# Kernel optimization log

Measured on AMD Instinct MI355X. Metric: run time of the kernel, lower is better.

The kernel has to match this reference:

```python
import jax, jax.numpy as jnp
import numpy as np

N_SP, N_SPAT = 20000, 10000
E_SS, E_BIP, E_SP = 160000, 320000, 320000
H, C = 4, 64  # GAT heads / per-head channels (hidden_channels=64, concat=False)
EPS = 1e-6


def _gat(xs, xd, row, col, ea, Ws, Wd, a_s, a_d, a_e, We, b, num_dst, heads, ch, self_loops, concat):
    # PyG GATConv with edge_dim: linear -> per-head additive attention -> softmax over incoming edges -> scatter-add
    hs = (xs @ Ws).reshape(-1, heads, ch)          # [Ns,H,C]
    hd = (xd @ Wd).reshape(-1, heads, ch)          # [Nd,H,C]
    al_s = jnp.sum(hs * a_s, -1)                   # [Ns,H]
    al_d = jnp.sum(hd * a_d, -1)                   # [Nd,H]
    if self_loops:
        # add_self_loops with fill_value='mean': loop edge_attr = mean of incoming edge_attr per node
        cnt = jax.ops.segment_sum(jnp.ones((row.shape[0],), ea.dtype), col, num_dst)
        loop_ea = jax.ops.segment_sum(ea, col, num_dst) / jnp.maximum(cnt, 1.0)[:, None]
        loops = jnp.arange(num_dst, dtype=row.dtype)
        row = jnp.concatenate([row, loops])
        col = jnp.concatenate([col, loops])
        ea = jnp.concatenate([ea, loop_ea], 0)
    he = (ea @ We).reshape(-1, heads, ch)          # [E,H,C]
    al = jax.nn.leaky_relu(al_s[row] + al_d[col] + jnp.sum(he * a_e, -1), 0.2)  # [E,H]
    m = jax.ops.segment_max(al, col, num_segments=num_dst)
    ex = jnp.exp(al - m[col])
    den = jax.ops.segment_sum(ex, col, num_segments=num_dst)
    alpha = ex / (den[col] + 1e-16)
    out = jax.ops.segment_sum(hs[row] * alpha[..., None], col, num_segments=num_dst)  # [Nd,H,C]
    out = out.reshape(num_dst, heads * ch) if concat else out.mean(1)
    return out + b


def setup_inputs() -> dict:
    key = jax.random.key(0)
    ks = iter(jax.random.split(key, 64))
    f = lambda shape: jax.random.normal(next(ks), shape, jnp.float32)
    w = lambda shape: f(shape) / np.sqrt(shape[0])
    inp = {}
    inp['species_x_mean'] = f((N_SP, 32))
    inp['species_x_std'] = jax.random.uniform(next(ks), (N_SP, 32), jnp.float32)
    inp['traits_nanmask'] = jax.random.bernoulli(next(ks), 0.4, (N_SP, 32))
    inp['species_x_gen'] = f((N_SP, 64))
    inp['species_x_phylo'] = f((N_SP, 128))
    inp['spatial_x'] = f((N_SPAT, 12))
    inp['spatial_global_data'] = f((N_SPAT, 4))
    ei = lambda e, ns, nd: jnp.stack([jax.random.randint(next(ks), (e,), 0, ns, jnp.int32),
                                      jax.random.randint(next(ks), (e,), 0, nd, jnp.int32)])
    inp['ss_edge_index'] = ei(E_SS, N_SPAT, N_SPAT)
    inp['ss_edge_attr'] = jax.random.uniform(next(ks), (E_SS, 1), jnp.float32)
    inp['bip_edge_index'] = ei(E_BIP, N_SPAT, N_SP)
    inp['bip_edge_attr'] = jax.random.uniform(next(ks), (E_BIP, 1), jnp.float32)
    inp['sp_edge_index'] = ei(E_SP, N_SP, N_SP)
    inp['sp_edge_attr'] = jax.random.uniform(next(ks), (E_SP, 1), jnp.float32)
    # GAT conv params: space_gnn (sg0, sg1), species_gnn (pg0, pg1)
    for nm, din in [('sg0', 16), ('sg1', 64), ('pg0', 128), ('pg1', 64)]:
        inp[nm + '_W'] = w((din, H * C))
        inp[nm + '_as'] = f((H, C)) * 0.1
        inp[nm + '_ad'] = f((H, C)) * 0.1
        inp[nm + '_ae'] = f((H, C)) * 0.1
        inp[nm + '_We'] = w((1, H * C))
        inp[nm + '_b'] = jnp.zeros((C,), jnp.float32)
    # bipartite GATConv: heads=1, concat=True, src dim=hidden=64, dst dim=in_gen+in_phylo=192
    inp['bp_Ws'] = w((64, 64))
    inp['bp_Wd'] = w((192, 64))
    inp['bp_as'] = f((1, 64)) * 0.1
    inp['bp_ad'] = f((1, 64)) * 0.1
    inp['bp_ae'] = f((1, 64)) * 0.1
    inp['bp_We'] = w((1, 64))
    inp['bp_b'] = jnp.zeros((64,), jnp.float32)
    inp['sl_W'] = w((288, 64))
    inp['sl_b'] = jnp.zeros((64,), jnp.float32)
    inp['fc_W'] = w((64, 64))
    inp['fc_b'] = jnp.zeros((64,), jnp.float32)
    return inp


def reference(species_x_mean, species_x_std, traits_nanmask, species_x_gen, species_x_phylo,
              spatial_x, spatial_global_data, ss_edge_index, ss_edge_attr, bip_edge_index,
              bip_edge_attr, sp_edge_index, sp_edge_attr,
              sg0_W, sg0_as, sg0_ad, sg0_ae, sg0_We, sg0_b,
              sg1_W, sg1_as, sg1_ad, sg1_ae, sg1_We, sg1_b,
              pg0_W, pg0_as, pg0_ad, pg0_ae, pg0_We, pg0_b,
              pg1_W, pg1_as, pg1_ad, pg1_ae, pg1_We, pg1_b,
              bp_Ws, bp_Wd, bp_as, bp_ad, bp_ae, bp_We, bp_b,
              sl_W, sl_b, fc_W, fc_b):
    # inference path: no trait masking -> visibility = observed mask
    vis = (~traits_nanmask).astype(jnp.float32)
    sp_in = jnp.concatenate([species_x_mean, species_x_std, vis, species_x_gen, species_x_phylo], 1)
    sp_in = jax.nn.relu(sp_in @ sl_W + sl_b)                      # [N_SP,64]
    # spatial GNN (2 GATConv layers, heads=4, concat=False, self loops)
    h = jnp.concatenate([spatial_x, spatial_global_data], 1)      # [N_SPAT,16]
    r, c = ss_edge_index[0], ss_edge_index[1]
    h = jax.nn.relu(_gat(h, h, r, c, ss_edge_attr, sg0_W, sg0_W, sg0_as, sg0_ad, sg0_ae, sg0_We, sg0_b, N_SPAT, H, C, True, False))
    h = jax.nn.relu(_gat(h, h, r, c, ss_edge_attr, sg1_W, sg1_W, sg1_as, sg1_ad, sg1_ae, sg1_We, sg1_b, N_SPAT, H, C, True, False))
    # bipartite spatial->species GATConv (heads=1, concat=True, no self loops)
    part = jnp.concatenate([species_x_gen, species_x_phylo], 1)   # [N_SP,192]
    br, bc = bip_edge_index[0], bip_edge_index[1]
    sts = jax.nn.relu(_gat(h, part, br, bc, bip_edge_attr, bp_Ws, bp_Wd, bp_as, bp_ad, bp_ae, bp_We, bp_b, N_SP, 1, 64, False, True))
    # species GNN (2 GATConv layers)
    x = jnp.concatenate([sts, sp_in], 1)                          # [N_SP,128]
    pr, pc = sp_edge_index[0], sp_edge_index[1]
    x = jax.nn.relu(_gat(x, x, pr, pc, sp_edge_attr, pg0_W, pg0_W, pg0_as, pg0_ad, pg0_ae, pg0_We, pg0_b, N_SP, H, C, True, False))
    x = jax.nn.relu(_gat(x, x, pr, pc, sp_edge_attr, pg1_W, pg1_W, pg1_as, pg1_ad, pg1_ae, pg1_We, pg1_b, N_SP, H, C, True, False))
    ms = x @ fc_W + fc_b                                          # [N_SP, 2*out]
    mean, log_std = jnp.split(ms, 2, axis=-1)
    std = jax.nn.softplus(log_std) + EPS
    return mean, std
```

## Files before the change

### kernel.cpp

```cpp
#include <hip/hip_runtime.h>
#include <hip/hip_bf16.h>

#define NSP   20000
#define NSPAT 10000
#define ESS   160000
#define EBIP  320000
#define ESP   320000

static inline int cdiv_host(long a, long b) { return (int)((a + b - 1) / b); }

__device__ __forceinline__ float wave_red_sum(float p) {
#pragma unroll
  for (int m = 32; m >= 1; m >>= 1) p += __shfl_xor(p, m, 64);
  return p;
}
__device__ __forceinline__ float bf2f(unsigned short u) {
  return __uint_as_float(((unsigned int)u) << 16);
}
__device__ __forceinline__ unsigned short f2bf(float f) {
  unsigned int u = __float_as_uint(f);
  unsigned int r = (u + 0x7FFF + ((u >> 16) & 1)) >> 16;
  return (unsigned short)r;
}

__global__ void count3_kernel(
    const int* c1, int E1, int* cp1, int* rnk1, int n1,
    const int* c2, int E2, int* cp2, int* rnk2, int n2,
    const int* c3, int E3, int* cp3, int* rnk3, int n3,
    const unsigned int* __restrict__ mask, int* __restrict__ flag) {
  int b = blockIdx.x, t = threadIdx.x;
  if (b == gridDim.x - 1) {
    if (t < 64) {
      unsigned int w0 = mask[t], w1 = mask[t + 64], w2 = mask[t + 128], w3 = mask[t + 192];
      bool ai = (w0 <= 1u) && (w1 <= 1u) && (w2 <= 1u) && (w3 <= 1u);
      auto okf = [](unsigned int w) { return w == 0u || w == 0x3f800000u; };
      bool af = okf(w0) && okf(w1) && okf(w2) && okf(w3);
      unsigned long long bi = __ballot(ai), bf = __ballot(af);
      if (t == 0) *flag = (bi == ~0ull) ? 0 : ((bf == ~0ull) ? 2 : 1);
    }
    return;
  }
  int i = b * 256 + t;
  int total = E1 + E2 + E3;
  if (i >= total) return;
  int p = (i >> 8) & 7;
  if (i < E1) {
    int d = c1[i]; rnk1[i] = atomicAdd(&cp1[p * n1 + d], 1);
  } else if (i < E1 + E2) {
    int j = i - E1;
    int d = c2[j]; rnk2[j] = atomicAdd(&cp2[p * n2 + d], 1);
  } else {
    int j = i - E1 - E2;
    int d = c3[j]; rnk3[j] = atomicAdd(&cp3[p * n3 + d], 1);
  }
}

__global__ void merge3_kernel(int* cp1, int* c1, int n1,
                              int* cp2, int* c2, int n2,
                              int* cp3, int* c3, int n3) {
  int i = blockIdx.x * blockDim.x + threadIdx.x;
  int total = n1 + n2 + n3;
  if (i >= total) return;
  int *cp, *c; int n, d;
  if (i < n1) { cp = cp1; c = c1; n = n1; d = i; }
  else if (i < n1 + n2) { cp = cp2; c = c2; n = n2; d = i - n1; }
  else { cp = cp3; c = c3; n = n3; d = i - n1 - n2; }
  int s = 0;
#pragma unroll
  for (int p = 0; p < 8; ++p) { int t = cp[p * n + d]; cp[p * n + d] = s; s += t; }
  c[d] = s;
}

__global__ __launch_bounds__(1024) void scan3_kernel(
    const int* cntA, int nA, int* ptrA,
    const int* cntB, int nB, int* ptrB,
    const int* cntC, int nC, int* ptrC) {
  const int* cnt; int n; int* ptr;
  if (blockIdx.x == 0) { cnt = cntA; n = nA; ptr = ptrA; }
  else if (blockIdx.x == 1) { cnt = cntB; n = nB; ptr = ptrB; }
  else { cnt = cntC; n = nC; ptr = ptrC; }
  __shared__ int part[1024];
  int t = threadIdx.x;
  int ch = (n + 1023) / 1024;
  int beg = t * ch, end = min(beg + ch, n);
  int s = 0;
  for (int i = beg; i < end; ++i) s += cnt[i];
  part[t] = s;
  __syncthreads();
  for (int off = 1; off < 1024; off <<= 1) {
    int v = (t >= off) ? part[t - off] : 0;
    __syncthreads();
    part[t] += v;
    __syncthreads();
  }
  int run = (t == 0) ? 0 : part[t - 1];
  for (int i = beg; i < end; ++i) { ptr[i] = run; run += cnt[i]; }
  if (t == 1023) ptr[n] = part[1023];
}

struct DoteArgs { const float* We[5]; const float* ae[5]; float* dotes; };
struct PrepArgs {
  const float* mean; const float* stdv; const void* mask; const int* flag;
  const float* sx; const float* sg; float* spc96; float* h0;
};

__global__ void scatter3x_kernel(
    const int* r1, const int* c1, const float* e1, int E1, const int* p1, const int* cp1, const int* k1, int n1, int* s1, float* a1,
    const int* r2, const int* c2, const float* e2, int E2, const int* p2, const int* cp2, const int* k2, int n2, int* s2, float* a2,
    const int* r3, const int* c3, const float* e3, int E3, const int* p3, const int* cp3, const int* k3, int n3, int* s3, float* a3,
    DoteArgs da, PrepArgs pa) {
  const int NB_SC = (ESS + EBIP + ESP + 255) / 256;
  int b = blockIdx.x, t = threadIdx.x;
  if (b < NB_SC) {
    int i = b * 256 + t;
    if (i >= E1 + E2 + E3) return;
    int p = (i >> 8) & 7;
    if (i < E1) {
      int d = c1[i];
      int pos = p1[d] + cp1[p * n1 + d] + k1[i];
      s1[pos] = r1[i]; a1[pos] = e1[i];
    } else if (i < E1 + E2) {
      int j = i - E1;
      int d = c2[j];
      int pos = p2[d] + cp2[p * n2 + d] + k2[j];
      s2[pos] = r2[j]; a2[pos] = e2[j];
    } else {
      int j = i - E1 - E2;
      int d = c3[j];
      int pos = p3[d] + cp3[p * n3 + d] + k3[j];
      s3[pos] = r3[j]; a3[pos] = e3[j];
    }
  } else if (b < NB_SC + 5) {
    int lb = b - NB_SC;
    int n = (lb == 2) ? 64 : 256;
    if (t < n) {
      float p = wave_red_sum(da.We[lb][t] * da.ae[lb][t]);
      if ((t & 63) == 0) da.dotes[lb * 4 + (t >> 6)] = p;
    }
  } else {
    const long totA = (long)NSP * 96;
    const long totB = (long)NSPAT * 16;
    long i = (long)(b - NB_SC - 5) * 256 + t;
    if (i >= totA + totB) return;
    int mode = *pa.flag;
    if (i < totA) {
      int n = (int)(i / 96), c = (int)(i % 96);
      float v;
      if (c < 32) v = pa.mean[(long)n * 32 + c];
      else if (c < 64) v = pa.stdv[(long)n * 32 + (c - 32)];
      else {
        long j = (long)n * 32 + (c - 64);
        int mv;
        if (mode == 0) mv = ((const int*)pa.mask)[j];
        else if (mode == 2) mv = (((const float*)pa.mask)[j] != 0.0f);
        else mv = (int)((const unsigned char*)pa.mask)[j];
        v = mv ? 0.f : 1.f;
      }
      pa.spc96[i] = v;
    } else {
      long k = i - totA;
      int n = (int)(k / 16), c = (int)(k % 16);
      pa.h0[k] = (c < 12) ? pa.sx[(long)n * 12 + c] : pa.sg[(long)n * 4 + (c - 12)];
    }
  }
}

struct XSrc { const float* p[5]; int w[5]; int n; };
struct PJob {
  XSrc xs; int M, K;
  const float* W; const float* bias; int mode;
  const float* a_s; const float* a_d;
  float* al_s; float* al_d;
  float* Y; float* Y2;
};
struct LeafArgs {
  const int* ss_ptr; const float* ss_cea; float* ss_lea;
  const int* pp_ptr; const float* pp_cea; float* pp_lea;
};

__device__ __forceinline__ void proj64_body(const PJob& J, int bid,
                                            float* wl, float* xl) {
  constexpr int KC = 32;
  constexpr int BR = 32;
  constexpr int KCP = 36;
  int t = threadIdx.x;
  long row0 = (long)bid * BR;
  if (row0 >= J.M) return;
  int cg = t & 15, rg = t >> 4;
  int c0 = cg * 4;

  float acc[2][4];
#pragma unroll
  for (int r = 0; r < 2; ++r)
#pragma unroll
    for (int j = 0; j < 4; ++j) acc[r][j] = 0.f;

  for (int k0 = 0; k0 < J.K; k0 += KC) {
    int seg = 0; int base = 0;
    while (k0 >= base + J.xs.w[seg]) { base += J.xs.w[seg]; ++seg; }
    const float* Xp = J.xs.p[seg];
    int stride = J.xs.w[seg];
    int kloc = k0 - base;

    __syncthreads();
    {
      const float4* ws = (const float4*)(J.W + (long)k0 * 64);
      float4* wd = (float4*)wl;
      wd[t] = ws[t];
      wd[t + 256] = ws[t + 256];
    }
    {
      int r = t >> 3, kq = (t & 7) * 4;
      long rr = row0 + r; if (rr >= J.M) rr = J.M - 1;
      float4 v = *(const float4*)(Xp + rr * stride + kloc + kq);
      *(float4*)(xl + r * KCP + kq) = v;
    }
    __syncthreads();

    for (int kg = 0; kg < KC; kg += 4) {
      float4 w0 = *(const float4*)(wl + (kg + 0) * 64 + c0);
      float4 w1 = *(const float4*)(wl + (kg + 1) * 64 + c0);
      float4 w2 = *(const float4*)(wl + (kg + 2) * 64 + c0);
      float4 w3 = *(const float4*)(wl + (kg + 3) * 64 + c0);
#pragma unroll
      for (int r = 0; r < 2; ++r) {
        float4 xv = *(const float4*)(xl + (rg * 2 + r) * KCP + kg);
        acc[r][0] = fmaf(xv.x, w0.x, acc[r][0]);
        acc[r][1] = fmaf(xv.x, w0.y, acc[r][1]);
        acc[r][2] = fmaf(xv.x, w0.z, acc[r][2]);
        acc[r][3] = fmaf(xv.x, w0.w, acc[r][3]);
        acc[r][0] = fmaf(xv.y, w1.x, acc[r][0]);
        acc[r][1] = fmaf(xv.y, w1.y, acc[r][1]);
        acc[r][2] = fmaf(xv.y, w1.z, acc[r][2]);
        acc[r][3] = fmaf(xv.y, w1.w, acc[r][3]);
        acc[r][0] = fmaf(xv.z, w2.x, acc[r][0]);
        acc[r][1] = fmaf(xv.z, w2.y, acc[r][1]);
        acc[r][2] = fmaf(xv.z, w2.z, acc[r][2]);
        acc[r][3] = fmaf(xv.z, w2.w, acc[r][3]);
        acc[r][0] = fmaf(xv.w, w3.x, acc[r][0]);
        acc[r][1] = fmaf(xv.w, w3.y, acc[r][1]);
        acc[r][2] = fmaf(xv.w, w3.z, acc[r][2]);
        acc[r][3] = fmaf(xv.w, w3.w, acc[r][3]);
      }
    }
  }

  float4 bv = make_float4(0.f, 0.f, 0.f, 0.f);
  float4 asv = make_float4(0.f, 0.f, 0.f, 0.f);
  float4 adv = make_float4(0.f, 0.f, 0.f, 0.f);
  if (J.bias) bv = *(const float4*)(J.bias + c0);
  if (J.a_s) asv = *(const float4*)(J.a_s + c0);
  if (J.a_d) adv = *(const float4*)(J.a_d + c0);

#pragma unroll
  for (int r = 0; r < 2; ++r) {
    long m = row0 + rg * 2 + r;
    bool ok = m < J.M;
    float v0 = acc[r][0] + bv.x, v1 = acc[r][1] + bv.y;
    float v2 = acc[r][2] + bv.z, v3 = acc[r][3] + bv.w;
    if (J.mode == 1) {
      if (ok)
        *(float4*)(J.Y + m * 64 + c0) = make_float4(
            fmaxf(v0, 0.f), fmaxf(v1, 0.f), fmaxf(v2, 0.f), fmaxf(v3, 0.f));
    } else if (J.mode == 2) {
      if (ok) {
        if (c0 < 32) {
          *(float4*)(J.Y + m * 32 + c0) = make_float4(v0, v1, v2, v3);
        } else {
          float4 o;
          o.x = fmaxf(v0, 0.f) + log1pf(__expf(-fabsf(v0))) + 1e-6f;
          o.y = fmaxf(v1, 0.f) + log1pf(__expf(-fabsf(v1))) + 1e-6f;
          o.z = fmaxf(v2, 0.f) + log1pf(__expf(-fabsf(v2))) + 1e-6f;
          o.w = fmaxf(v3, 0.f) + log1pf(__expf(-fabsf(v3))) + 1e-6f;
          *(float4*)(J.Y2 + m * 32 + (c0 - 32)) = o;
        }
      }
    } else if (ok && J.Y) {
      *(float4*)(J.Y + m * 64 + c0) = make_float4(v0, v1, v2, v3);
    }
    if (J.a_s) {
      float s = acc[r][0] * asv.x + acc[r][1] * asv.y + acc[r][2] * asv.z + acc[r][3] * asv.w;
      s += __shfl_xor(s, 1); s += __shfl_xor(s, 2);
      s += __shfl_xor(s, 4); s += __shfl_xor(s, 8);
      if (ok && cg == 0) J.al_s[m] = s;
    }
    if (J.a_d) {
      float s = acc[r][0] * adv.x + acc[r][1] * adv.y + acc[r][2] * adv.z + acc[r][3] * adv.w;
      s += __shfl_xor(s, 1); s += __shfl_xor(s, 2);
      s += __shfl_xor(s, 4); s += __shfl_xor(s, 8);
      if (ok && cg == 0) J.al_d[m] = s;
    }
  }
}

__global__ __launch_bounds__(256) void proj64x2l_kernel(PJob j0, PJob j1,
                                                        int nb0, int nb1,
                                                        LeafArgs la) {
  __shared__ float wl[32 * 64];
  __shared__ float xl[32 * 36];
  int b = blockIdx.x, t = threadIdx.x;
  if (b < nb0) {
    proj64_body(j0, b, wl, xl);
  } else if (b < nb0 + nb1) {
    proj64_body(j1, b - nb0, wl, xl);
  } else {
    int i = (b - nb0 - nb1) * 256 + t;
    if (i >= NSPAT + NSP) return;
    const int* ptr; const float* cea; float* lea; int d;
    if (i < NSPAT) { ptr = la.ss_ptr; cea = la.ss_cea; lea = la.ss_lea; d = i; }
    else { ptr = la.pp_ptr; cea = la.pp_cea; lea = la.pp_lea; d = i - NSPAT; }
    int e0 = ptr[d], e1 = ptr[d + 1];
    float s = 0.f;
    for (int e = e0; e < e1; ++e) s += cea[e];
    lea[d] = s / (float)max(e1 - e0, 1);
  }
}

__global__ __launch_bounds__(256) void proj_kernel(
    XSrc xsrc, int M, int K,
    const float* __restrict__ W,
    const float* __restrict__ a_s, const float* __restrict__ a_d,
    float* __restrict__ al_s, float* __restrict__ al_d,
    unsigned short* __restrict__ Y) {
  constexpr int KC = 32;
  constexpr int RPT = 8;
  constexpr int BR = 32;
  constexpr int KCP = 36;
  constexpr int H = 4;
  __shared__ float wl[KC * 256];
  __shared__ float xl[BR * KCP];

  int t = threadIdx.x;
  int cg = t & 63, rg = t >> 6;
  int c0 = cg * 4;
  long row0 = (long)blockIdx.x * BR;

  float acc[RPT][4];
#pragma unroll
  for (int r = 0; r < RPT; ++r)
#pragma unroll
    for (int j = 0; j < 4; ++j) acc[r][j] = 0.f;

  for (int k0 = 0; k0 < K; k0 += KC) {
    int kc = min(KC, K - k0);
    int seg = 0; int base = 0;
    while (k0 >= base + xsrc.w[seg]) { base += xsrc.w[seg]; ++seg; }
    const float* Xp = xsrc.p[seg];
    int stride = xsrc.w[seg];
    int kloc = k0 - base;

    __syncthreads();
    {
      const float4* wsrc = (const float4*)(W + (long)k0 * 256);
      float4* wdst = (float4*)wl;
      for (int i = t; i < (kc * 256) >> 2; i += 256) wdst[i] = wsrc[i];
    }
    for (int i = t; i < BR * 8; i += 256) {
      int r = i >> 3, kq = (i & 7) * 4;
      if (kq < kc) {
        long rr = row0 + r; if (rr >= M) rr = M - 1;
        float4 v = *(const float4*)(Xp + rr * stride + kloc + kq);
        *(float4*)(xl + r * KCP + kq) = v;
      }
    }
    __syncthreads();

    for (int kg = 0; kg < kc; kg += 4) {
      float4 w0 = *(const float4*)(wl + (kg + 0) * 256 + c0);
      float4 w1 = *(const float4*)(wl + (kg + 1) * 256 + c0);
      float4 w2 = *(const float4*)(wl + (kg + 2) * 256 + c0);
      float4 w3 = *(const float4*)(wl + (kg + 3) * 256 + c0);
      float4 xv[RPT];
#pragma unroll
      for (int r = 0; r < RPT; ++r)
        xv[r] = *(const float4*)(xl + (rg * RPT + r) * KCP + kg);
#pragma unroll
      for (int r = 0; r < RPT; ++r) {
        acc[r][0] = fmaf(xv[r].x, w0.x, acc[r][0]);
        acc[r][1] = fmaf(xv[r].x, w0.y, acc[r][1]);
        acc[r][2] = fmaf(xv[r].x, w0.z, acc[r][2]);
        acc[r][3] = fmaf(xv[r].x, w0.w, acc[r][3]);
        acc[r][0] = fmaf(xv[r].y, w1.x, acc[r][0]);
        acc[r][1] = fmaf(xv[r].y, w1.y, acc[r][1]);
        acc[r][2] = fmaf(xv[r].y, w1.z, acc[r][2]);
        acc[r][3] = fmaf(xv[r].y, w1.w, acc[r][3]);
        acc[r][0] = fmaf(xv[r].z, w2.x, acc[r][0]);
        acc[r][1] = fmaf(xv[r].z, w2.y, acc[r][1]);
        acc[r][2] = fmaf(xv[r].z, w2.z, acc[r][2]);
        acc[r][3] = fmaf(xv[r].z, w2.w, acc[r][3]);
        acc[r][0] = fmaf(xv[r].w, w3.x, acc[r][0]);
        acc[r][1] = fmaf(xv[r].w, w3.y, acc[r][1]);
        acc[r][2] = fmaf(xv[r].w, w3.z, acc[r][2]);
        acc[r][3] = fmaf(xv[r].w, w3.w, acc[r][3]);
      }
    }
  }

  float4 asv = *(const float4*)(a_s + c0);
  float4 adv = *(const float4*)(a_d + c0);

#pragma unroll
  for (int r = 0; r < RPT; ++r) {
    long m = row0 + (long)rg * RPT + r;
    bool ok = m < M;
    if (ok) {
      ushort4 o;
      o.x = f2bf(acc[r][0]); o.y = f2bf(acc[r][1]);
      o.z = f2bf(acc[r][2]); o.w = f2bf(acc[r][3]);
      *(ushort4*)(Y + m * 256 + c0) = o;
    }
    float s = acc[r][0] * asv.x + acc[r][1] * asv.y + acc[r][2] * asv.z + acc[r][3] * asv.w;
    s += __shfl_xor(s, 1); s += __shfl_xor(s, 2);
    s += __shfl_xor(s, 4); s += __shfl_xor(s, 8);
    if (ok && (cg & 15) == 0) al_s[m * H + (c0 >> 6)] = s;
    float d = acc[r][0] * adv.x + acc[r][1] * adv.y + acc[r][2] * adv.z + acc[r][3] * adv.w;
    d += __shfl_xor(d, 1); d += __shfl_xor(d, 2);
    d += __shfl_xor(d, 4); d += __shfl_xor(d, 8);
    if (ok && (cg & 15) == 0) al_d[m * H + (c0 >> 6)] = d;
  }
}

__device__ __forceinline__ void fma4_bf(float4& a, float al, ushort4 u) {
  a.x = fmaf(al, bf2f(u.x), a.x); a.y = fmaf(al, bf2f(u.y), a.y);
  a.z = fmaf(al, bf2f(u.z), a.z); a.w = fmaf(al, bf2f(u.w), a.w);
}
__device__ __forceinline__ void scale4(float4& a, float s) {
  a.x *= s; a.y *= s; a.z *= s; a.w *= s;
}

template <bool SELFLOOP>
__global__ __launch_bounds__(256) void gat4_fused(
    int Nd, const int* __restrict__ dptr, const int* __restrict__ csr_src,
    const float* __restrict__ csr_ea, const float* __restrict__ al_s,
    const float* __restrict__ al_d, const float* __restrict__ dote,
    const float* __restrict__ loop_ea, const unsigned short* __restrict__ hs,
    const float* __restrict__ bias, float* __restrict__ out) {
  int wave = threadIdx.x >> 6, lane = threadIdx.x & 63;
  int n = blockIdx.x * 4 + wave;
  if (n >= Nd) return;
  int h = lane >> 4;
  float ald = al_d[(long)n * 4 + h];
  float de = dote[h];
  int e0 = dptr[n], e1 = dptr[n + 1];
  float m0 = -INFINITY, d0 = 0.f;
  float4 a0 = make_float4(0.f, 0.f, 0.f, 0.f);
  if (SELFLOOP) {
    float l = al_s[(long)n * 4 + h] + ald + loop_ea[n] * de;
    l = (l > 0.f) ? l : 0.2f * l;
    m0 = l; d0 = 1.f;
    ushort4 u = *(const ushort4*)(hs + (long)n * 256 + lane * 4);
    a0.x = bf2f(u.x); a0.y = bf2f(u.y); a0.z = bf2f(u.z); a0.w = bf2f(u.w);
  }
  float m1 = -INFINITY, d1 = 0.f;
  float4 a1 = make_float4(0.f, 0.f, 0.f, 0.f);
  int e = e0;
  for (; e + 2 <= e1; e += 2) {
    int s0 = csr_src[e], s1 = csr_src[e + 1];
    float l0 = al_s[(long)s0 * 4 + h] + ald + csr_ea[e] * de;
    float l1 = al_s[(long)s1 * 4 + h] + ald + csr_ea[e + 1] * de;
    l0 = (l0 > 0.f) ? l0 : 0.2f * l0;
    l1 = (l1 > 0.f) ? l1 : 0.2f * l1;
    ushort4 u0 = *(const ushort4*)(hs + (long)s0 * 256 + lane * 4);
    ushort4 u1 = *(const ushort4*)(hs + (long)s1 * 256 + lane * 4);
    if (l0 > m0) { float sc = __expf(m0 - l0); d0 *= sc; scale4(a0, sc); m0 = l0; }
    float ex0 = __expf(l0 - m0);
    d0 += ex0;
    fma4_bf(a0, ex0, u0);
    if (l1 > m1) { float sc = __expf(m1 - l1); d1 *= sc; scale4(a1, sc); m1 = l1; }
    float ex1 = __expf(l1 - m1);
    d1 += ex1;
    fma4_bf(a1, ex1, u1);
  }
  if (e < e1) {
    int s0 = csr_src[e];
    float l0 = al_s[(long)s0 * 4 + h] + ald + csr_ea[e] * de;
    l0 = (l0 > 0.f) ? l0 : 0.2f * l0;
    ushort4 u0 = *(const ushort4*)(hs + (long)s0 * 256 + lane * 4);
    if (l0 > m0) { float sc = __expf(m0 - l0); d0 *= sc; scale4(a0, sc); m0 = l0; }
    float ex0 = __expf(l0 - m0);
    d0 += ex0;
    fma4_bf(a0, ex0, u0);
  }
  if (m1 != -INFINITY) {
    float M = fmaxf(m0, m1);
    float sA = (m0 == -INFINITY) ? 0.f : __expf(m0 - M);
    float sB = __expf(m1 - M);
    d0 = d0 * sA + d1 * sB;
    a0.x = a0.x * sA + a1.x * sB; a0.y = a0.y * sA + a1.y * sB;
    a0.z = a0.z * sA + a1.z * sB; a0.w = a0.w * sA + a1.w * sB;
  }
  float inv = 1.f / (d0 + 1e-16f);
  scale4(a0, inv);
  a0.x += __shfl_xor(a0.x, 16); a0.y += __shfl_xor(a0.y, 16);
  a0.z += __shfl_xor(a0.z, 16); a0.w += __shfl_xor(a0.w, 16);
  a0.x += __shfl_xor(a0.x, 32); a0.y += __shfl_xor(a0.y, 32);
  a0.z += __shfl_xor(a0.z, 32); a0.w += __shfl_xor(a0.w, 32);
  if (lane < 16) {
    float4 b = *(const float4*)(bias + lane * 4);
    float4 o;
    o.x = fmaxf(a0.x * 0.25f + b.x, 0.f);
    o.y = fmaxf(a0.y * 0.25f + b.y, 0.f);
    o.z = fmaxf(a0.z * 0.25f + b.z, 0.f);
    o.w = fmaxf(a0.w * 0.25f + b.w, 0.f);
    *(float4*)(out + (long)n * 64 + lane * 4) = o;
  }
}

__global__ __launch_bounds__(256) void gat1_fused(
    int Nd, const int* __restrict__ dptr, const int* __restrict__ csr_src,
    const float* __restrict__ csr_ea, const float* __restrict__ al_s,
    const float* __restrict__ al_d, const float* __restrict__ dote,
    const float* __restrict__ hs, const float* __restrict__ bias,
    float* __restrict__ out) {
  int wave = threadIdx.x >> 6, lane = threadIdx.x & 63;
  int n = blockIdx.x * 4 + wave;
  if (n >= Nd) return;
  float ald = al_d[n];
  float de = dote[0];
  int e0 = dptr[n], e1 = dptr[n + 1];
  float m0 = -INFINITY, d0 = 0.f, acc0 = 0.f;
  float m1 = -INFINITY, d1 = 0.f, acc1 = 0.f;
  int e = e0;
  for (; e + 2 <= e1; e += 2) {
    int s0 = csr_src[e], s1 = csr_src[e + 1];
    float l0 = al_s[s0] + ald + csr_ea[e] * de;
    float l1 = al_s[s1] + ald + csr_ea[e + 1] * de;
    l0 = (l0 > 0.f) ? l0 : 0.2f * l0;
    l1 = (l1 > 0.f) ? l1 : 0.2f * l1;
    float h0 = hs[(long)s0 * 64 + lane];
    float h1 = hs[(long)s1 * 64 + lane];
    if (l0 > m0) { float sc = __expf(m0 - l0); d0 *= sc; acc0 *= sc; m0 = l0; }
    float ex0 = __expf(l0 - m0);
    d0 += ex0; acc0 = fmaf(ex0, h0, acc0);
    if (l1 > m1) { float sc = __expf(m1 - l1); d1 *= sc; acc1 *= sc; m1 = l1; }
    float ex1 = __expf(l1 - m1);
    d1 += ex1; acc1 = fmaf(ex1, h1, acc1);
  }
  if (e < e1) {
    int s0 = csr_src[e];
    float l0 = al_s[s0] + ald + csr_ea[e] * de;
    l0 = (l0 > 0.f) ? l0 : 0.2f * l0;
    float h0 = hs[(long)s0 * 64 + lane];
    if (l0 > m0) { float sc = __expf(m0 - l0); d0 *= sc; acc0 *= sc; m0 = l0; }
    float ex0 = __expf(l0 - m0);
    d0 += ex0; acc0 = fmaf(ex0, h0, acc0);
  }
  if (m1 != -INFINITY) {
    float M = fmaxf(m0, m1);
    float sA = (m0 == -INFINITY) ? 0.f : __expf(m0 - M);
    float sB = __expf(m1 - M);
    d0 = d0 * sA + d1 * sB;
    acc0 = acc0 * sA + acc1 * sB;
  }
  float o = acc0 / (d0 + 1e-16f);
  out[(long)n * 64 + lane] = fmaxf(o + bias[lane], 0.f);
}

extern "C" void kernel_launch(void* const* d_in, const int* in_sizes, int n_in,
                              void* d_out, int out_size, void* d_ws, size_t ws_size,
                              hipStream_t stream) {
  const float* sp_mean = (const float*)d_in[0];
  const float* sp_std  = (const float*)d_in[1];
  const void*  nanmask = d_in[2];
  const float* sp_gen  = (const float*)d_in[3];
  const float* sp_phy  = (const float*)d_in[4];
  const float* spat_x  = (const float*)d_in[5];
  const float* spat_g  = (const float*)d_in[6];
  const int*   ss_ei   = (const int*)d_in[7];
  const float* ss_ea   = (const float*)d_in[8];
  const int*   bip_ei  = (const int*)d_in[9];
  const float* bip_ea  = (const float*)d_in[10];
  const int*   sp_ei   = (const int*)d_in[11];
  const float* sp_ea   = (const float*)d_in[12];
  const float* sg0_W = (const float*)d_in[13]; const float* sg0_as = (const float*)d_in[14];
  const float* sg0_ad = (const float*)d_in[15]; const float* sg0_ae = (const float*)d_in[16];
  const float* sg0_We = (const float*)d_in[17]; const float* sg0_b = (const float*)d_in[18];
  const float* sg1_W = (const float*)d_in[19]; const float* sg1_as = (const float*)d_in[20];
  const float* sg1_ad = (const float*)d_in[21]; const float* sg1_ae = (const float*)d_in[22];
  const float* sg1_We = (const float*)d_in[23]; const float* sg1_b = (const float*)d_in[24];
  const float* pg0_W = (const float*)d_in[25]; const float* pg0_as = (const float*)d_in[26];
  const float* pg0_ad = (const float*)d_in[27]; const float* pg0_ae = (const float*)d_in[28];
  const float* pg0_We = (const float*)d_in[29]; const float* pg0_b = (const float*)d_in[30];
  const float* pg1_W = (const float*)d_in[31]; const float* pg1_as = (const float*)d_in[32];
  const float* pg1_ad = (const float*)d_in[33]; const float* pg1_ae = (const float*)d_in[34];
  const float* pg1_We = (const float*)d_in[35]; const float* pg1_b = (const float*)d_in[36];
  const float* bp_Ws = (const float*)d_in[37]; const float* bp_Wd = (const float*)d_in[38];
  const float* bp_as = (const float*)d_in[39]; const float* bp_ad = (const float*)d_in[40];
  const float* bp_ae = (const float*)d_in[41]; const float* bp_We = (const float*)d_in[42];
  const float* bp_b  = (const float*)d_in[43];
  const float* sl_W  = (const float*)d_in[44]; const float* sl_b  = (const float*)d_in[45];
  const float* fc_W  = (const float*)d_in[46]; const float* fc_b  = (const float*)d_in[47];

  char* wsb = (char*)d_ws;
  size_t off = 0;
  auto A = [&](size_t nbytes) -> void* {
    void* p = wsb + off;
    off += (nbytes + 255) & ~(size_t)255;
    return p;
  };
  int* ss_cp = (int*)A((size_t)8 * NSPAT * 4);
  int* bp_cp = (int*)A((size_t)8 * NSP * 4);
  int* pp_cp = (int*)A((size_t)8 * NSP * 4);
  size_t zbytes = off;
  int*   ss_cnt = (int*)A((NSPAT + 1) * 4);
  int*   bp_cnt = (int*)A((NSP + 1) * 4);
  int*   pp_cnt = (int*)A((NSP + 1) * 4);
  int*   flag  = (int*)A(4);
  float* dotes = (float*)A(5 * 4 * sizeof(float));
  float* alS   = (float*)A((size_t)NSP * 4 * 4);
  float* alD   = (float*)A((size_t)NSP * 4 * 4);
  float* alSb  = (float*)A((size_t)NSPAT * 4);
  float* alDb  = (float*)A((size_t)NSP * 4);
  float* spc96 = (float*)A((size_t)NSP * 96 * 4);
  float* sp_in = (float*)A((size_t)NSP * 64 * 4);
  float* h0    = (float*)A((size_t)NSPAT * 16 * 4);
  float* h_a   = (float*)A((size_t)NSPAT * 64 * 4);
  float* h_b   = (float*)A((size_t)NSPAT * 64 * 4);
  float* HS    = (float*)A((size_t)NSP * 256 * 4);
  float* sts   = (float*)A((size_t)NSP * 64 * 4);
  float* x1    = (float*)A((size_t)NSP * 64 * 4);
  int*   ss_ptr = (int*)A((NSPAT + 1) * 4);
  int*   ss_src = (int*)A((size_t)ESS * 4);
  float* ss_cea = (float*)A((size_t)ESS * 4);
  int*   ss_rnk = (int*)A((size_t)ESS * 4);
  float* ss_lea = (float*)A((size_t)NSPAT * 4);
  int*   bp_ptr = (int*)A((NSP + 1) * 4);
  int*   bp_src = (int*)A((size_t)EBIP * 4);
  float* bp_cea = (float*)A((size_t)EBIP * 4);
  int*   bp_rnk = (int*)A((size_t)EBIP * 4);
  int*   pp_ptr = (int*)A((NSP + 1) * 4);
  int*   pp_src = (int*)A((size_t)ESP * 4);
  float* pp_cea = (float*)A((size_t)ESP * 4);
  int*   pp_rnk = (int*)A((size_t)ESP * 4);
  float* pp_lea = (float*)A((size_t)NSP * 4);
  (void)ws_size; (void)in_sizes; (void)n_in; (void)out_size;

  const int TB = 256;
  hipMemsetAsync(wsb, 0, zbytes, stream);

  count3_kernel<<<cdiv_host(ESS + EBIP + ESP, TB) + 1, TB, 0, stream>>>(
      ss_ei + ESS, ESS, ss_cp, ss_rnk, NSPAT,
      bip_ei + EBIP, EBIP, bp_cp, bp_rnk, NSP,
      sp_ei + ESP, ESP, pp_cp, pp_rnk, NSP,
      (const unsigned int*)nanmask, flag);
  merge3_kernel<<<cdiv_host(NSPAT + NSP + NSP, TB), TB, 0, stream>>>(
      ss_cp, ss_cnt, NSPAT, bp_cp, bp_cnt, NSP, pp_cp, pp_cnt, NSP);
  scan3_kernel<<<3, 1024, 0, stream>>>(ss_cnt, NSPAT, ss_ptr, bp_cnt, NSP, bp_ptr, pp_cnt, NSP, pp_ptr);

  {
    DoteArgs da{};
    da.We[0] = sg0_We; da.ae[0] = sg0_ae;
    da.We[1] = sg1_We; da.ae[1] = sg1_ae;
    da.We[2] = bp_We;  da.ae[2] = bp_ae;
    da.We[3] = pg0_We; da.ae[3] = pg0_ae;
    da.We[4] = pg1_We; da.ae[4] = pg1_ae;
    da.dotes = dotes;
    PrepArgs pa{ sp_mean, sp_std, nanmask, flag, spat_x, spat_g, spc96, h0 };
    int nb = cdiv_host(ESS + EBIP + ESP, TB) + 5 +
             cdiv_host((long)NSP * 96 + (long)NSPAT * 16, TB);
    scatter3x_kernel<<<nb, TB, 0, stream>>>(
        ss_ei, ss_ei + ESS, ss_ea, ESS, ss_ptr, ss_cp, ss_rnk, NSPAT, ss_src, ss_cea,
        bip_ei, bip_ei + EBIP, bip_ea, EBIP, bp_ptr, bp_cp, bp_rnk, NSP, bp_src, bp_cea,
        sp_ei, sp_ei + ESP, sp_ea, ESP, pp_ptr, pp_cp, pp_rnk, NSP, pp_src, pp_cea,
        da, pa);
  }

  {
    PJob j0{}; j0.xs.p[0] = spc96; j0.xs.w[0] = 96; j0.xs.p[1] = sp_gen; j0.xs.w[1] = 64;
    j0.xs.p[2] = sp_phy; j0.xs.w[2] = 128; j0.xs.n = 3;
    j0.M = NSP; j0.K = 288; j0.W = sl_W; j0.bias = sl_b; j0.mode = 1; j0.Y = sp_in;
    PJob j1{}; j1.xs.p[0] = sp_gen; j1.xs.w[0] = 64; j1.xs.p[1] = sp_phy; j1.xs.w[1] = 128;
    j1.xs.n = 2;
    j1.M = NSP; j1.K = 192; j1.W = bp_Wd; j1.mode = 0; j1.a_d = bp_ad; j1.al_d = alDb;
    LeafArgs la{ ss_ptr, ss_cea, ss_lea, pp_ptr, pp_cea, pp_lea };
    int nb0 = cdiv_host(NSP, 32), nb1 = cdiv_host(NSP, 32);
    int nbl = cdiv_host(NSPAT + NSP, TB);
    proj64x2l_kernel<<<nb0 + nb1 + nbl, TB, 0, stream>>>(j0, j1, nb0, nb1, la);
  }

  {
    XSrc xs{}; xs.p[0] = h0; xs.w[0] = 16; xs.n = 1;
    proj_kernel<<<cdiv_host(NSPAT, 32), TB, 0, stream>>>(xs, NSPAT, 16, sg0_W,
        sg0_as, sg0_ad, alS, alD, (unsigned short*)HS);
  }
  gat4_fused<true><<<cdiv_host(NSPAT, 4), TB, 0, stream>>>(
      NSPAT, ss_ptr, ss_src, ss_cea, alS, alD, dotes + 0, ss_lea,
      (const unsigned short*)HS, sg0_b, h_a);
  {
    XSrc xs{}; xs.p[0] = h_a; xs.w[0] = 64; xs.n = 1;
    proj_kernel<<<cdiv_host(NSPAT, 32), TB, 0, stream>>>(xs, NSPAT, 64, sg1_W,
        sg1_as, sg1_ad, alS, alD, (unsigned short*)HS);
  }
  gat4_fused<true><<<cdiv_host(NSPAT, 4), TB, 0, stream>>>(
      NSPAT, ss_ptr, ss_src, ss_cea, alS, alD, dotes + 4, ss_lea,
      (const unsigned short*)HS, sg1_b, h_b);

  {
    PJob j0{}; j0.xs.p[0] = h_b; j0.xs.w[0] = 64; j0.xs.n = 1;
    j0.M = NSPAT; j0.K = 64; j0.W = bp_Ws; j0.mode = 0;
    j0.a_s = bp_as; j0.al_s = alSb; j0.Y = h_a;
    LeafArgs la{ ss_ptr, ss_cea, ss_lea, pp_ptr, pp_cea, pp_lea };
    int nb0 = cdiv_host(NSPAT, 32);
    proj64x2l_kernel<<<nb0, TB, 0, stream>>>(j0, j0, nb0, 0, la);
  }
  gat1_fused<<<cdiv_host(NSP, 4), TB, 0, stream>>>(
      NSP, bp_ptr, bp_src, bp_cea, alSb, alDb, dotes + 8, h_a, bp_b, sts);

  {
    XSrc xs{}; xs.p[0] = sts; xs.w[0] = 64; xs.p[1] = sp_in; xs.w[1] = 64; xs.n = 2;
    proj_kernel<<<cdiv_host(NSP, 32), TB, 0, stream>>>(xs, NSP, 128, pg0_W,
        pg0_as, pg0_ad, alS, alD, (unsigned short*)HS);
  }
  gat4_fused<true><<<cdiv_host(NSP, 4), TB, 0, stream>>>(
      NSP, pp_ptr, pp_src, pp_cea, alS, alD, dotes + 12, pp_lea,
      (const unsigned short*)HS, pg0_b, x1);
  {
    XSrc xs{}; xs.p[0] = x1; xs.w[0] = 64; xs.n = 1;
    proj_kernel<<<cdiv_host(NSP, 32), TB, 0, stream>>>(xs, NSP, 64, pg1_W,
        pg1_as, pg1_ad, alS, alD, (unsigned short*)HS);
  }
  gat4_fused<true><<<cdiv_host(NSP, 4), TB, 0, stream>>>(
      NSP, pp_ptr, pp_src, pp_cea, alS, alD, dotes + 16, pp_lea,
      (const unsigned short*)HS, pg1_b, sts);

  {
    PJob j0{}; j0.xs.p[0] = sts; j0.xs.w[0] = 64; j0.xs.n = 1;
    j0.M = NSP; j0.K = 64; j0.W = fc_W; j0.bias = fc_b; j0.mode = 2;
    j0.Y = (float*)d_out; j0.Y2 = (float*)d_out + (long)NSP * 32;
    LeafArgs la{ ss_ptr, ss_cea, ss_lea, pp_ptr, pp_cea, pp_lea };
    int nb0 = cdiv_host(NSP, 32);
    proj64x2l_kernel<<<nb0, TB, 0, stream>>>(j0, j0, nb0, 0, la);
  }
}
```

Baseline: 488.6 us.

## Fuse CSR merge+scan, unroll GAT edge loops to 4, fuse final GAT with FC head

The per-partition count layout changes from partition-major to node-major (d*8+p), so the merge and prefix scan fold into one kernel and one launch plus the count buffers go away. The GAT edge aggregation loops in gat4 and gat1 now keep four independent online-softmax accumulators instead of two, which exposes more memory-level parallelism on the gathers. The last species GAT layer is fused with the final linear and softplus head through a shared-memory copy of fc_W, dropping one kernel and the round trip of the hidden features. Each block now loads fc_W into shared memory, and the single-block-per-graph scan kernel does more serial work per thread.

```diff
diff --git a/kernel.cpp b/kernel.cpp
--- a/kernel.cpp
+++ b/kernel.cpp
@@ -45,46 +45,33 @@
   if (i >= total) return;
   int p = (i >> 8) & 7;
   if (i < E1) {
-    int d = c1[i]; rnk1[i] = atomicAdd(&cp1[p * n1 + d], 1);
+    int d = c1[i]; rnk1[i] = atomicAdd(&cp1[d * 8 + p], 1);
   } else if (i < E1 + E2) {
     int j = i - E1;
-    int d = c2[j]; rnk2[j] = atomicAdd(&cp2[p * n2 + d], 1);
+    int d = c2[j]; rnk2[j] = atomicAdd(&cp2[d * 8 + p], 1);
   } else {
     int j = i - E1 - E2;
-    int d = c3[j]; rnk3[j] = atomicAdd(&cp3[p * n3 + d], 1);
-  }
-}
-
-__global__ void merge3_kernel(int* cp1, int* c1, int n1,
-                              int* cp2, int* c2, int n2,
-                              int* cp3, int* c3, int n3) {
-  int i = blockIdx.x * blockDim.x + threadIdx.x;
-  int total = n1 + n2 + n3;
-  if (i >= total) return;
-  int *cp, *c; int n, d;
-  if (i < n1) { cp = cp1; c = c1; n = n1; d = i; }
-  else if (i < n1 + n2) { cp = cp2; c = c2; n = n2; d = i - n1; }
-  else { cp = cp3; c = c3; n = n3; d = i - n1 - n2; }
-  int s = 0;
-#pragma unroll
-  for (int p = 0; p < 8; ++p) { int t = cp[p * n + d]; cp[p * n + d] = s; s += t; }
-  c[d] = s;
-}
-
-__global__ __launch_bounds__(1024) void scan3_kernel(
-    const int* cntA, int nA, int* ptrA,
-    const int* cntB, int nB, int* ptrB,
-    const int* cntC, int nC, int* ptrC) {
-  const int* cnt; int n; int* ptr;
-  if (blockIdx.x == 0) { cnt = cntA; n = nA; ptr = ptrA; }
-  else if (blockIdx.x == 1) { cnt = cntB; n = nB; ptr = ptrB; }
-  else { cnt = cntC; n = nC; ptr = ptrC; }
+    int d = c3[j]; rnk3[j] = atomicAdd(&cp3[d * 8 + p], 1);
+  }
+}
+
+__global__ __launch_bounds__(1024) void mergescan3_kernel(
+    int* cpA, int nA, int* ptrA,
+    int* cpB, int nB, int* ptrB,
+    int* cpC, int nC, int* ptrC) {
+  int* cp; int n; int* ptr;
+  if (blockIdx.x == 0) { cp = cpA; n = nA; ptr = ptrA; }
+  else if (blockIdx.x == 1) { cp = cpB; n = nB; ptr = ptrB; }
+  else { cp = cpC; n = nC; ptr = ptrC; }
   __shared__ int part[1024];
   int t = threadIdx.x;
   int ch = (n + 1023) / 1024;
   int beg = t * ch, end = min(beg + ch, n);
   int s = 0;
-  for (int i = beg; i < end; ++i) s += cnt[i];
+  for (int d = beg; d < end; ++d) {
+#pragma unroll
+    for (int p = 0; p < 8; ++p) s += cp[d * 8 + p];
+  }
   part[t] = s;
   __syncthreads();
   for (int off = 1; off < 1024; off <<= 1) {
@@ -94,7 +81,13 @@
     __syncthreads();
   }
   int run = (t == 0) ? 0 : part[t - 1];
-  for (int i = beg; i < end; ++i) { ptr[i] = run; run += cnt[i]; }
+  for (int d = beg; d < end; ++d) {
+    ptr[d] = run;
+    int acc = 0;
+#pragma unroll
+    for (int p = 0; p < 8; ++p) { int v = cp[d * 8 + p]; cp[d * 8 + p] = acc; acc += v; }
+    run += acc;
+  }
   if (t == 1023) ptr[n] = part[1023];
 }
 
@@ -117,17 +110,17 @@
     int p = (i >> 8) & 7;
     if (i < E1) {
       int d = c1[i];
-      int pos = p1[d] + cp1[p * n1 + d] + k1[i];
+      int pos = p1[d] + cp1[d * 8 + p] + k1[i];
       s1[pos] = r1[i]; a1[pos] = e1[i];
     } else if (i < E1 + E2) {
       int j = i - E1;
       int d = c2[j];
-      int pos = p2[d] + cp2[p * n2 + d] + k2[j];
+      int pos = p2[d] + cp2[d * 8 + p] + k2[j];
       s2[pos] = r2[j]; a2[pos] = e2[j];
     } else {
       int j = i - E1 - E2;
       int d = c3[j];
-      int pos = p3[d] + cp3[p * n3 + d] + k3[j];
+      int pos = p3[d] + cp3[d * 8 + p] + k3[j];
       s3[pos] = r3[j]; a3[pos] = e3[j];
     }
   } else if (b < NB_SC + 5) {
@@ -428,6 +421,83 @@
   a.x *= s; a.y *= s; a.z *= s; a.w *= s;
 }
 
+struct OS4 { float m, d; float4 a; };
+__device__ __forceinline__ void os4_init(OS4& o) {
+  o.m = -INFINITY; o.d = 0.f; o.a = make_float4(0.f, 0.f, 0.f, 0.f);
+}
+__device__ __forceinline__ void os4_upd(OS4& o, float l, ushort4 u) {
+  if (l > o.m) { float sc = __expf(o.m - l); o.d *= sc; scale4(o.a, sc); o.m = l; }
+  float ex = __expf(l - o.m);
+  o.d += ex; fma4_bf(o.a, ex, u);
+}
+__device__ __forceinline__ void os4_mrg(OS4& A, const OS4& B) {
+  if (B.m == -INFINITY) return;
+  if (A.m == -INFINITY) { A = B; return; }
+  float M = fmaxf(A.m, B.m);
+  float sA = __expf(A.m - M), sB = __expf(B.m - M);
+  A.d = A.d * sA + B.d * sB;
+  A.a.x = A.a.x * sA + B.a.x * sB;
+  A.a.y = A.a.y * sA + B.a.y * sB;
+  A.a.z = A.a.z * sA + B.a.z * sB;
+  A.a.w = A.a.w * sA + B.a.w * sB;
+  A.m = M;
+}
+
+template <bool SELFLOOP>
+__device__ __forceinline__ float4 gat4_body(
+    int n, int lane, const int* __restrict__ dptr, const int* __restrict__ csr_src,
+    const float* __restrict__ csr_ea, const float* __restrict__ al_s,
+    const float* __restrict__ al_d, const float* __restrict__ dote,
+    const float* __restrict__ loop_ea, const unsigned short* __restrict__ hs) {
+  int h = lane >> 4;
+  float ald = al_d[(long)n * 4 + h];
+  float de = dote[h];
+  int e0 = dptr[n], e1 = dptr[n + 1];
+  OS4 o0, o1, o2, o3;
+  os4_init(o0); os4_init(o1); os4_init(o2); os4_init(o3);
+  if (SELFLOOP) {
+    float l = al_s[(long)n * 4 + h] + ald + loop_ea[n] * de;
+    l = (l > 0.f) ? l : 0.2f * l;
+    o0.m = l; o0.d = 1.f;
+    ushort4 u = *(const ushort4*)(hs + (long)n * 256 + lane * 4);
+    o0.a.x = bf2f(u.x); o0.a.y = bf2f(u.y); o0.a.z = bf2f(u.z); o0.a.w = bf2f(u.w);
+  }
+  int e = e0;
+  for (; e + 4 <= e1; e += 4) {
+    int s0 = csr_src[e], s1 = csr_src[e + 1], s2 = csr_src[e + 2], s3 = csr_src[e + 3];
+    float l0 = al_s[(long)s0 * 4 + h] + ald + csr_ea[e] * de;
+    float l1 = al_s[(long)s1 * 4 + h] + ald + csr_ea[e + 1] * de;
+    float l2 = al_s[(long)s2 * 4 + h] + ald + csr_ea[e + 2] * de;
+    float l3 = al_s[(long)s3 * 4 + h] + ald + csr_ea[e + 3] * de;
+    ushort4 u0 = *(const ushort4*)(hs + (long)s0 * 256 + lane * 4);
+    ushort4 u1 = *(const ushort4*)(hs + (long)s1 * 256 + lane * 4);
+    ushort4 u2 = *(const ushort4*)(hs + (long)s2 * 256 + lane * 4);
+    ushort4 u3 = *(const ushort4*)(hs + (long)s3 * 256 + lane * 4);
+    l0 = (l0 > 0.f) ? l0 : 0.2f * l0;
+    l1 = (l1 > 0.f) ? l1 : 0.2f * l1;
+    l2 = (l2 > 0.f) ? l2 : 0.2f * l2;
+    l3 = (l3 > 0.f) ? l3 : 0.2f * l3;
+    os4_upd(o0, l0, u0); os4_upd(o1, l1, u1);
+    os4_upd(o2, l2, u2); os4_upd(o3, l3, u3);
+  }
+  for (; e < e1; ++e) {
+    int s0 = csr_src[e];
+    float l0 = al_s[(long)s0 * 4 + h] + ald + csr_ea[e] * de;
+    l0 = (l0 > 0.f) ? l0 : 0.2f * l0;
+    ushort4 u0 = *(const ushort4*)(hs + (long)s0 * 256 + lane * 4);
+    os4_upd(o0, l0, u0);
+  }
+  os4_mrg(o0, o1); os4_mrg(o2, o3); os4_mrg(o0, o2);
+  float inv = 1.f / (o0.d + 1e-16f);
+  scale4(o0.a, inv);
+  float4 a0 = o0.a;
+  a0.x += __shfl_xor(a0.x, 16); a0.y += __shfl_xor(a0.y, 16);
+  a0.z += __shfl_xor(a0.z, 16); a0.w += __shfl_xor(a0.w, 16);
+  a0.x += __shfl_xor(a0.x, 32); a0.y += __shfl_xor(a0.y, 32);
+  a0.z += __shfl_xor(a0.z, 32); a0.w += __shfl_xor(a0.w, 32);
+  return a0;
+}
+
 template <bool SELFLOOP>
 __global__ __launch_bounds__(256) void gat4_fused(
     int Nd, const int* __restrict__ dptr, const int* __restrict__ csr_src,
@@ -438,63 +508,8 @@
   int wave = threadIdx.x >> 6, lane = threadIdx.x & 63;
   int n = blockIdx.x * 4 + wave;
   if (n >= Nd) return;
-  int h = lane >> 4;
-  float ald = al_d[(long)n * 4 + h];
-  float de = dote[h];
-  int e0 = dptr[n], e1 = dptr[n + 1];
-  float m0 = -INFINITY, d0 = 0.f;
-  float4 a0 = make_float4(0.f, 0.f, 0.f, 0.f);
-  if (SELFLOOP) {
-    float l = al_s[(long)n * 4 + h] + ald + loop_ea[n] * de;
-    l = (l > 0.f) ? l : 0.2f * l;
-    m0 = l; d0 = 1.f;
-    ushort4 u = *(const ushort4*)(hs + (long)n * 256 + lane * 4);
-    a0.x = bf2f(u.x); a0.y = bf2f(u.y); a0.z = bf2f(u.z); a0.w = bf2f(u.w);
-  }
-  float m1 = -INFINITY, d1 = 0.f;
-  float4 a1 = make_float4(0.f, 0.f, 0.f, 0.f);
-  int e = e0;
-  for (; e + 2 <= e1; e += 2) {
-    int s0 = csr_src[e], s1 = csr_src[e + 1];
-    float l0 = al_s[(long)s0 * 4 + h] + ald + csr_ea[e] * de;
-    float l1 = al_s[(long)s1 * 4 + h] + ald + csr_ea[e + 1] * de;
-    l0 = (l0 > 0.f) ? l0 : 0.2f * l0;
-    l1 = (l1 > 0.f) ? l1 : 0.2f * l1;
-    ushort4 u0 = *(const ushort4*)(hs + (long)s0 * 256 + lane * 4);
-    ushort4 u1 = *(const ushort4*)(hs + (long)s1 * 256 + lane * 4);
-    if (l0 > m0) { float sc = __expf(m0 - l0); d0 *= sc; scale4(a0, sc); m0 = l0; }
-    float ex0 = __expf(l0 - m0);
-    d0 += ex0;
-    fma4_bf(a0, ex0, u0);
-    if (l1 > m1) { float sc = __expf(m1 - l1); d1 *= sc; scale4(a1, sc); m1 = l1; }
-    float ex1 = __expf(l1 - m1);
-    d1 += ex1;
-    fma4_bf(a1, ex1, u1);
-  }
-  if (e < e1) {
-    int s0 = csr_src[e];
-    float l0 = al_s[(long)s0 * 4 + h] + ald + csr_ea[e] * de;
-    l0 = (l0 > 0.f) ? l0 : 0.2f * l0;
-    ushort4 u0 = *(const ushort4*)(hs + (long)s0 * 256 + lane * 4);
-    if (l0 > m0) { float sc = __expf(m0 - l0); d0 *= sc; scale4(a0, sc); m0 = l0; }
-    float ex0 = __expf(l0 - m0);
-    d0 += ex0;
-    fma4_bf(a0, ex0, u0);
-  }
-  if (m1 != -INFINITY) {
-    float M = fmaxf(m0, m1);
-    float sA = (m0 == -INFINITY) ? 0.f : __expf(m0 - M);
-    float sB = __expf(m1 - M);
-    d0 = d0 * sA + d1 * sB;
-    a0.x = a0.x * sA + a1.x * sB; a0.y = a0.y * sA + a1.y * sB;
-    a0.z = a0.z * sA + a1.z * sB; a0.w = a0.w * sA + a1.w * sB;
-  }
-  float inv = 1.f / (d0 + 1e-16f);
-  scale4(a0, inv);
-  a0.x += __shfl_xor(a0.x, 16); a0.y += __shfl_xor(a0.y, 16);
-  a0.z += __shfl_xor(a0.z, 16); a0.w += __shfl_xor(a0.w, 16);
-  a0.x += __shfl_xor(a0.x, 32); a0.y += __shfl_xor(a0.y, 32);
-  a0.z += __shfl_xor(a0.z, 32); a0.w += __shfl_xor(a0.w, 32);
+  float4 a0 = gat4_body<SELFLOOP>(n, lane, dptr, csr_src, csr_ea, al_s, al_d,
+                                  dote, loop_ea, hs);
   if (lane < 16) {
     float4 b = *(const float4*)(bias + lane * 4);
     float4 o;
@@ -504,6 +519,67 @@
     o.w = fmaxf(a0.w * 0.25f + b.w, 0.f);
     *(float4*)(out + (long)n * 64 + lane * 4) = o;
   }
+}
+
+__global__ __launch_bounds__(256) void gat4_fc(
+    int Nd, const int* __restrict__ dptr, const int* __restrict__ csr_src,
+    const float* __restrict__ csr_ea, const float* __restrict__ al_s,
+    const float* __restrict__ al_d, const float* __restrict__ dote,
+    const float* __restrict__ loop_ea, const unsigned short* __restrict__ hs,
+    const float* __restrict__ bias, const float* __restrict__ fcW,
+    const float* __restrict__ fcb, float* __restrict__ meanO,
+    float* __restrict__ stdO) {
+  __shared__ float Wl[64 * 64];
+  int t = threadIdx.x;
+  {
+    const float4* ws = (const float4*)fcW;
+    float4* wd = (float4*)Wl;
+    wd[t] = ws[t]; wd[t + 256] = ws[t + 256];
+    wd[t + 512] = ws[t + 512]; wd[t + 768] = ws[t + 768];
+  }
+  __syncthreads();
+  int wave = t >> 6, lane = t & 63;
+  int n = blockIdx.x * 4 + wave;
+  if (n >= Nd) return;
+  float4 a0 = gat4_body<true>(n, lane, dptr, csr_src, csr_ea, al_s, al_d,
+                              dote, loop_ea, hs);
+  float4 b = *(const float4*)(bias + (lane & 15) * 4);
+  float4 o;
+  o.x = fmaxf(a0.x * 0.25f + b.x, 0.f);
+  o.y = fmaxf(a0.y * 0.25f + b.y, 0.f);
+  o.z = fmaxf(a0.z * 0.25f + b.z, 0.f);
+  o.w = fmaxf(a0.w * 0.25f + b.w, 0.f);
+  float accf = 0.f;
+#pragma unroll
+  for (int q = 0; q < 16; ++q) {
+    float vx = __shfl(o.x, q), vy = __shfl(o.y, q);
+    float vz = __shfl(o.z, q), vw = __shfl(o.w, q);
+    accf = fmaf(vx, Wl[(4 * q + 0) * 64 + lane], accf);
+    accf = fmaf(vy, Wl[(4 * q + 1) * 64 + lane], accf);
+    accf = fmaf(vz, Wl[(4 * q + 2) * 64 + lane], accf);
+    accf = fmaf(vw, Wl[(4 * q + 3) * 64 + lane], accf);
+  }
+  float v = accf + fcb[lane];
+  if (lane < 32) {
+    meanO[(long)n * 32 + lane] = v;
+  } else {
+    stdO[(long)n * 32 + (lane - 32)] =
+        fmaxf(v, 0.f) + log1pf(__expf(-fabsf(v))) + 1e-6f;
+  }
+}
+
+__device__ __forceinline__ void os1_upd(float& m, float& d, float& c, float l, float hv) {
+  if (l > m) { float sc = __expf(m - l); d *= sc; c *= sc; m = l; }
+  float ex = __expf(l - m);
+  d += ex; c = fmaf(ex, hv, c);
+}
+__device__ __forceinline__ void os1_mrg(float& m0, float& d0, float& c0,
+                                        float m1, float d1, float c1) {
+  if (m1 == -INFINITY) return;
+  if (m0 == -INFINITY) { m0 = m1; d0 = d1; c0 = c1; return; }
+  float M = fmaxf(m0, m1);
+  float sA = __expf(m0 - M), sB = __expf(m1 - M);
+  d0 = d0 * sA + d1 * sB; c0 = c0 * sA + c1 * sB; m0 = M;
 }
 
 __global__ __launch_bounds__(256) void gat1_fused(
@@ -518,41 +594,39 @@
   float ald = al_d[n];
   float de = dote[0];
   int e0 = dptr[n], e1 = dptr[n + 1];
-  float m0 = -INFINITY, d0 = 0.f, acc0 = 0.f;
-  float m1 = -INFINITY, d1 = 0.f, acc1 = 0.f;
+  float m0 = -INFINITY, d0 = 0.f, c0 = 0.f;
+  float m1 = -INFINITY, d1 = 0.f, c1 = 0.f;
+  float m2 = -INFINITY, d2 = 0.f, c2 = 0.f;
+  float m3 = -INFINITY, d3 = 0.f, c3 = 0.f;
   int e = e0;
-  for (; e + 2 <= e1; e += 2) {
-    int s0 = csr_src[e], s1 = csr_src[e + 1];
+  for (; e + 4 <= e1; e += 4) {
+    int s0 = csr_src[e], s1 = csr_src[e + 1], s2 = csr_src[e + 2], s3 = csr_src[e + 3];
     float l0 = al_s[s0] + ald + csr_ea[e] * de;
     float l1 = al_s[s1] + ald + csr_ea[e + 1] * de;
+    float l2 = al_s[s2] + ald + csr_ea[e + 2] * de;
+    float l3 = al_s[s3] + ald + csr_ea[e + 3] * de;
+    float h0 = hs[(long)s0 * 64 + lane];
+    float h1 = hs[(long)s1 * 64 + lane];
+    float h2 = hs[(long)s2 * 64 + lane];
+    float h3 = hs[(long)s3 * 64 + lane];
     l0 = (l0 > 0.f) ? l0 : 0.2f * l0;
     l1 = (l1 > 0.f) ? l1 : 0.2f * l1;
-    float h0 = hs[(long)s0 * 64 + lane];
-    float h1 = hs[(long)s1 * 64 + lane];
-    if (l0 > m0) { float sc = __expf(m0 - l0); d0 *= sc; acc0 *= sc; m0 = l0; }
-    float ex0 = __expf(l0 - m0);
-    d0 += ex0; acc0 = fmaf(ex0, h0, acc0);
-    if (l1 > m1) { float sc = __expf(m1 - l1); d1 *= sc; acc1 *= sc; m1 = l1; }
-    float ex1 = __expf(l1 - m1);
-    d1 += ex1; acc1 = fmaf(ex1, h1, acc1);
-  }
-  if (e < e1) {
+    l2 = (l2 > 0.f) ? l2 : 0.2f * l2;
+    l3 = (l3 > 0.f) ? l3 : 0.2f * l3;
+    os1_upd(m0, d0, c0, l0, h0); os1_upd(m1, d1, c1, l1, h1);
+    os1_upd(m2, d2, c2, l2, h2); os1_upd(m3, d3, c3, l3, h3);
+  }
+  for (; e < e1; ++e) {
     int s0 = csr_src[e];
     float l0 = al_s[s0] + ald + csr_ea[e] * de;
     l0 = (l0 > 0.f) ? l0 : 0.2f * l0;
     float h0 = hs[(long)s0 * 64 + lane];
-    if (l0 > m0) { float sc = __expf(m0 - l0); d0 *= sc; acc0 *= sc; m0 = l0; }
-    float ex0 = __expf(l0 - m0);
-    d0 += ex0; acc0 = fmaf(ex0, h0, acc0);
-  }
-  if (m1 != -INFINITY) {
-    float M = fmaxf(m0, m1);
-    float sA = (m0 == -INFINITY) ? 0.f : __expf(m0 - M);
-    float sB = __expf(m1 - M);
-    d0 = d0 * sA + d1 * sB;
-    acc0 = acc0 * sA + acc1 * sB;
-  }
-  float o = acc0 / (d0 + 1e-16f);
+    os1_upd(m0, d0, c0, l0, h0);
+  }
+  os1_mrg(m0, d0, c0, m1, d1, c1);
+  os1_mrg(m2, d2, c2, m3, d3, c3);
+  os1_mrg(m0, d0, c0, m2, d2, c2);
+  float o = c0 / (d0 + 1e-16f);
   out[(long)n * 64 + lane] = fmaxf(o + bias[lane], 0.f);
 }
 
@@ -602,9 +676,6 @@
   int* bp_cp = (int*)A((size_t)8 * NSP * 4);
   int* pp_cp = (int*)A((size_t)8 * NSP * 4);
   size_t zbytes = off;
-  int*   ss_cnt = (int*)A((NSPAT + 1) * 4);
-  int*   bp_cnt = (int*)A((NSP + 1) * 4);
-  int*   pp_cnt = (int*)A((NSP + 1) * 4);
   int*   flag  = (int*)A(4);
   float* dotes = (float*)A(5 * 4 * sizeof(float));
   float* alS   = (float*)A((size_t)NSP * 4 * 4);
@@ -643,9 +714,9 @@
       bip_ei + EBIP, EBIP, bp_cp, bp_rnk, NSP,
       sp_ei + ESP, ESP, pp_cp, pp_rnk, NSP,
       (const unsigned int*)nanmask, flag);
-  merge3_kernel<<<cdiv_host(NSPAT + NSP + NSP, TB), TB, 0, stream>>>(
-      ss_cp, ss_cnt, NSPAT, bp_cp, bp_cnt, NSP, pp_cp, pp_cnt, NSP);
-  scan3_kernel<<<3, 1024, 0, stream>>>(ss_cnt, NSPAT, ss_ptr, bp_cnt, NSP, bp_ptr, pp_cnt, NSP, pp_ptr);
+  mergescan3_kernel<<<3, 1024, 0, stream>>>(ss_cp, NSPAT, ss_ptr,
+                                            bp_cp, NSP, bp_ptr,
+                                            pp_cp, NSP, pp_ptr);
 
   {
     DoteArgs da{};
@@ -719,16 +790,8 @@
     proj_kernel<<<cdiv_host(NSP, 32), TB, 0, stream>>>(xs, NSP, 64, pg1_W,
         pg1_as, pg1_ad, alS, alD, (unsigned short*)HS);
   }
-  gat4_fused<true><<<cdiv_host(NSP, 4), TB, 0, stream>>>(
+  gat4_fc<<<cdiv_host(NSP, 4), TB, 0, stream>>>(
       NSP, pp_ptr, pp_src, pp_cea, alS, alD, dotes + 16, pp_lea,
-      (const unsigned short*)HS, pg1_b, sts);
-
-  {
-    PJob j0{}; j0.xs.p[0] = sts; j0.xs.w[0] = 64; j0.xs.n = 1;
-    j0.M = NSP; j0.K = 64; j0.W = fc_W; j0.bias = fc_b; j0.mode = 2;
-    j0.Y = (float*)d_out; j0.Y2 = (float*)d_out + (long)NSP * 32;
-    LeafArgs la{ ss_ptr, ss_cea, ss_lea, pp_ptr, pp_cea, pp_lea };
-    int nb0 = cdiv_host(NSP, 32);
-    proj64x2l_kernel<<<nb0, TB, 0, stream>>>(j0, j0, nb0, 0, la);
-  }
-}
+      (const unsigned short*)HS, pg1_b, fc_W, fc_b,
+      (float*)d_out, (float*)d_out + (long)NSP * 32);
+}
```

Measured after the change: 528.0 us. 8.1% more time.
